# Kernel tuning notes

Measured on AMD Instinct MI355X. Metric: run time of the kernel, lower is better.

## Reference

```python
import jax, jax.numpy as jnp
import numpy as np
import math

N_EMBD = 1024
N_HEAD = 16
HEAD_DIM = N_EMBD // N_HEAD


def setup_inputs() -> dict:
    key = jax.random.key(0)
    k_x, k_w1, k_b1, k_w2, k_b2 = jax.random.split(key, 5)
    B, T = 2, 2048
    x = jax.random.normal(k_x, (B, T, N_EMBD), dtype=jnp.float32)
    # ln1: Linear(n_embd, 3*n_embd); weights stored as [in, out] for x @ W
    W_qkv = jax.random.normal(k_w1, (N_EMBD, 3 * N_EMBD), dtype=jnp.float32) * 0.02
    b_qkv = jax.random.normal(k_b1, (3 * N_EMBD,), dtype=jnp.float32) * 0.02
    # ln2: Linear(n_embd, n_embd)
    W_out = jax.random.normal(k_w2, (N_EMBD, N_EMBD), dtype=jnp.float32) * 0.02
    b_out = jax.random.normal(k_b2, (N_EMBD,), dtype=jnp.float32) * 0.02
    return {"x": x, "W_qkv": W_qkv, "b_qkv": b_qkv, "W_out": W_out, "b_out": b_out}


def reference(x, W_qkv, b_qkv, W_out, b_out):
    B, T, C = x.shape
    qkv = x @ W_qkv + b_qkv                      # [B,T,3C]
    q, k, v = jnp.split(qkv, 3, axis=-1)
    # reshape to heads: [B, H, T, D]
    def to_heads(t):
        return t.reshape(B, T, N_HEAD, HEAD_DIM).transpose(0, 2, 1, 3)
    Q, K, V = to_heads(q), to_heads(k), to_heads(v)
    # NOTE: scale is 1/sqrt(n_head), as in the source (not sqrt(head_dim));
    # NOTE: no causal mask is applied, faithfully matching the source forward.
    scale = 1.0 / math.sqrt(N_HEAD)
    scores = jnp.einsum('bhqd,bhkd->bhqk', Q, K) * scale  # [B,H,T,T]
    attn = jax.nn.softmax(scores, axis=-1)
    out = jnp.einsum('bhqk,bhkd->bhqd', attn, V)          # [B,H,T,D]
    out = out.transpose(0, 2, 1, 3).reshape(B, T, C)
    # dropout = 0.0 -> identity (eval mode)
    return out @ W_out + b_out
```

## Files before the change

kernel.cpp:

```cpp
#include <hip/hip_runtime.h>
#include <hip/hip_bf16.h>
#include <stdint.h>

typedef __bf16 bf16_t;
typedef __bf16 bf16x8 __attribute__((ext_vector_type(8)));
typedef float  f32x4  __attribute__((ext_vector_type(4)));

#define AS1 __attribute__((address_space(1)))
#define AS3 __attribute__((address_space(3)))

__device__ __forceinline__ void gload16(const bf16_t* g, char* l) {
  __builtin_amdgcn_global_load_lds((AS1 const void*)(uintptr_t)g, (AS3 void*)l, 16, 0, 0);
}
__device__ __forceinline__ int swz8(int r) { return (r & 7) ^ ((r >> 2) & 6); }

#define C2S 0.36067376022224085f

__global__ __launch_bounds__(256) void prep(
    const float* __restrict__ x, const float* __restrict__ Wqkv, const float* __restrict__ Wout,
    bf16_t* __restrict__ xb, bf16_t* __restrict__ wqkvT, bf16_t* __restrict__ woutT) {
  __shared__ float tile[32][33];
  const int bid = blockIdx.x, tid = threadIdx.x;
  if (bid < 4096) {
    const int i = bid * 256 + tid;
    float4 v = reinterpret_cast<const float4*>(x)[i];
    union { bf16_t h[4]; unsigned long long u; } r;
    r.h[0] = (bf16_t)v.x; r.h[1] = (bf16_t)v.y; r.h[2] = (bf16_t)v.z; r.h[3] = (bf16_t)v.w;
    reinterpret_cast<unsigned long long*>(xb)[i] = r.u;
    return;
  }
  const float* W; bf16_t* Wt; int N, tb;
  if (bid < 7168) { W = Wqkv; Wt = wqkvT; N = 3072; tb = bid - 4096; }
  else            { W = Wout; Wt = woutT; N = 1024; tb = bid - 7168; }
  const int kb = (tb & 31) * 32, nb = (tb >> 5) * 32;
  const int tx = tid & 31, ty = tid >> 5;
#pragma unroll
  for (int i = 0; i < 32; i += 8)
    tile[ty + i][tx] = W[(size_t)(kb + ty + i) * N + nb + tx];
  __syncthreads();
  const int r = tid >> 3;
  const int c0 = (tid & 7) * 4;
  union { bf16_t h4[4]; unsigned long long u; } pk;
#pragma unroll
  for (int j = 0; j < 4; ++j) pk.h4[j] = (bf16_t)tile[c0 + j][r];
  *reinterpret_cast<unsigned long long*>(&Wt[(size_t)(nb + r) * 1024 + kb + c0]) = pk.u;
}

__global__ __launch_bounds__(512) void gemm8(
    const bf16_t* __restrict__ A, const bf16_t* __restrict__ Bt,
    const float* __restrict__ bias,
    bf16_t* __restrict__ outb, bf16_t* __restrict__ vtb,
    int N, int K, int ldo) {
  __shared__ bf16_t lA[3][4096];
  __shared__ bf16_t lB[3][4096];
  const int tid = threadIdx.x;
  const int wave = tid >> 6, lane = tid & 63;
  const int lr = lane & 15, lg = lane >> 4;
  const int ntiles = N >> 7;
  int bm, bn;
  if (ntiles == 24) {
    const int xcd = blockIdx.x & 7, l = blockIdx.x >> 3;
    bm = (xcd >> 1) * 8 + (l & 7);
    bn = (xcd & 1) * 12 + (l >> 3);
  } else {
    const int bid = (blockIdx.x & 7) * ((int)gridDim.x >> 3) + (blockIdx.x >> 3);
    bn = bid % ntiles; bm = bid / ntiles;
  }
  const int m0 = bm * 128, n0 = bn * 128;
  const int wr = wave >> 2, wc = wave & 3;
  f32x4 acc[4][2] = {};

  const int srow = tid >> 2;
  const int scolb = ((tid & 3) << 4) ^ (((srow >> 1) & 3) << 4);
  const bf16_t* Asrc = A  + (size_t)(m0 + srow) * K + (scolb >> 1);
  const bf16_t* Bsrc = Bt + (size_t)(n0 + srow) * K + (scolb >> 1);
  auto stage = [&](int buf, int k0) {
    gload16(Asrc + k0, (char*)&lA[buf][0] + wave * 1024);
    gload16(Bsrc + k0, (char*)&lB[buf][0] + wave * 1024);
  };

  auto ldA = [&](const char* p, int mi) {
    const int row = wr * 64 + mi * 16 + lr;
    return *reinterpret_cast<const bf16x8*>(p + row * 64 + ((lg * 16) ^ (((row >> 1) & 3) << 4)));
  };
  auto ldB = [&](const char* p, int ni) {
    const int row = wc * 32 + ni * 16 + lr;
    return *reinterpret_cast<const bf16x8*>(p + row * 64 + ((lg * 16) ^ (((row >> 1) & 3) << 4)));
  };

  const int nt = K >> 5;
  stage(0, 0);
  stage(1, 32);
  int cur = 0, stg = 2;

  for (int t = 0; t < nt; ++t) {
    if (t + 2 < nt) {
      stage(stg, (t + 2) << 5);
      asm volatile("s_waitcnt vmcnt(4)" ::: "memory");
    } else if (t + 1 < nt) {
      asm volatile("s_waitcnt vmcnt(2)" ::: "memory");
    } else {
      asm volatile("s_waitcnt vmcnt(0)" ::: "memory");
    }
    __builtin_amdgcn_s_barrier();
    __builtin_amdgcn_sched_barrier(0);

    const char* pA = (const char*)&lA[cur][0];
    const char* pB = (const char*)&lB[cur][0];
    bf16x8 af[4], bfv[2];
#pragma unroll
    for (int mi = 0; mi < 4; ++mi) af[mi] = ldA(pA, mi);
    bfv[0] = ldB(pB, 0); bfv[1] = ldB(pB, 1);

    __builtin_amdgcn_s_setprio(1);
#pragma unroll
    for (int mi = 0; mi < 4; ++mi)
#pragma unroll
      for (int ni = 0; ni < 2; ++ni)
        acc[mi][ni] = __builtin_amdgcn_mfma_f32_16x16x32_bf16(af[mi], bfv[ni], acc[mi][ni], 0, 0, 0);
    __builtin_amdgcn_s_setprio(0);

    __builtin_amdgcn_sched_barrier(0);
    __builtin_amdgcn_s_barrier();
    cur = cur == 2 ? 0 : cur + 1;
    stg = stg == 2 ? 0 : stg + 1;
  }

#pragma unroll
  for (int mi = 0; mi < 4; ++mi) {
#pragma unroll
    for (int ni = 0; ni < 2; ++ni) {
      const int col = n0 + wc * 32 + ni * 16 + lr;
      const float bv = bias[col];
      const int rg0 = m0 + wr * 64 + mi * 16 + lg * 4;
      if (col >= 2048) {
        const int colv = col - 2048;
        const int dd = colv & 63, hh = colv >> 6;
        const int bb = rg0 >> 11, t = rg0 & 2047;
        union { bf16_t h4[4]; unsigned long long u; } pk;
#pragma unroll
        for (int r = 0; r < 4; ++r) pk.h4[r] = (bf16_t)(acc[mi][ni][r] + bv);
        *reinterpret_cast<unsigned long long*>(
            vtb + (size_t)(bb * 16 + hh) * 131072 + (size_t)dd * 2048 + t) = pk.u;
      } else {
        const float sc = (col < 1024) ? C2S : 1.f;
#pragma unroll
        for (int r = 0; r < 4; ++r) {
          const float v = (acc[mi][ni][r] + bv) * sc;
          outb[(size_t)(rg0 + r) * ldo + col] = (bf16_t)v;
        }
      }
    }
  }
}

__global__ __launch_bounds__(512) void attn_fwd(
    const bf16_t* __restrict__ qkv2,
    const bf16_t* __restrict__ vT,
    bf16_t* __restrict__ a0, bf16_t* __restrict__ a1,
    float* __restrict__ lbuf) {
  __shared__ bf16_t lds[4][8192];
  const int tid = threadIdx.x;
  const int wave = tid >> 6, lane = tid & 63;
  const int lr = lane & 15, lg = lane >> 4;
  const int id = blockIdx.x;
  const int xcd = id & 7, slot = id >> 3;
  const int bh = xcd * 4 + (slot & 3);
  const int rest = slot >> 2;
  const int qb = rest & 7, kvh = rest >> 3;
  const int b = bh >> 4, h = bh & 15;

  const int q0 = qb * 256 + wave * 32;
  const bf16_t* Qp = qkv2 + (size_t)(b * 2048 + q0) * 2048 + h * 64;
  bf16x8 qf[2][2];
#pragma unroll
  for (int hx = 0; hx < 2; ++hx) {
    qf[hx][0] = *reinterpret_cast<const bf16x8*>(Qp + (size_t)(hx * 16 + lr) * 2048 + lg * 8);
    qf[hx][1] = *reinterpret_cast<const bf16x8*>(Qp + (size_t)(hx * 16 + lr) * 2048 + 32 + lg * 8);
  }

  const int kr = tid >> 3;
  const int ks = (tid & 7) ^ swz8(kr);
  const bf16_t* Ksrc = qkv2 + (size_t)(b * 2048 + kvh * 1024 + kr) * 2048 + 1024 + h * 64 + ks * 8;
  const bf16_t* Vsrc = vT + (size_t)bh * 131072 + (size_t)kr * 2048 + kvh * 1024 + ks * 8;

  auto stage = [&](int buf, int kb) {
    char* base = (char*)&lds[buf][0] + wave * 1024;
    gload16(Ksrc + (size_t)kb * 131072, base);
    gload16(Vsrc + (size_t)kb * 64, base + 8192);
  };

  int kofs[4][2], vofs[4][2];
#pragma unroll
  for (int t = 0; t < 4; ++t) {
    const int kk = 32 * (t >> 1) + 8 * (lr >> 2) + 4 * (t & 1) + (lr & 3);
    const int sw = swz8(kk) << 4;
    kofs[t][0] = (kk << 7) + ((lg * 16) ^ sw);
    kofs[t][1] = (kk << 7) + ((64 + lg * 16) ^ sw);
  }
#pragma unroll
  for (int nc = 0; nc < 4; ++nc) {
    const int vr = nc * 16 + lr;
    const int sw = swz8(vr) << 4;
    vofs[nc][0] = 8192 + (vr << 7) + ((lg * 16) ^ sw);
    vofs[nc][1] = 8192 + (vr << 7) + ((64 + lg * 16) ^ sw);
  }

  f32x4 acc[2][4] = {};
  f32x4 accl[2] = {};
  bf16x8 ones;
#pragma unroll
  for (int j = 0; j < 8; ++j) ones[j] = (bf16_t)1.0f;

  stage(0, 0);
  stage(1, 1);

  for (int kb = 0; kb < 16; ++kb) {
    const int cur = kb & 3;
    if (kb + 2 < 16) {
      stage((kb + 2) & 3, kb + 2);
      asm volatile("s_waitcnt vmcnt(4)" ::: "memory");
    } else if (kb + 1 < 16) {
      asm volatile("s_waitcnt vmcnt(2)" ::: "memory");
    } else {
      asm volatile("s_waitcnt vmcnt(0)" ::: "memory");
    }
    __builtin_amdgcn_s_barrier();
    __builtin_amdgcn_sched_barrier(0);
    const char* bK = (const char*)&lds[cur][0];

    f32x4 s[2][4];
#pragma unroll
    for (int t = 0; t < 4; ++t) {
      const bf16x8 k0 = *reinterpret_cast<const bf16x8*>(bK + kofs[t][0]);
      const bf16x8 k1 = *reinterpret_cast<const bf16x8*>(bK + kofs[t][1]);
#pragma unroll
      for (int hx = 0; hx < 2; ++hx) {
        f32x4 z = {0.f, 0.f, 0.f, 0.f};
        z = __builtin_amdgcn_mfma_f32_16x16x32_bf16(k0, qf[hx][0], z, 0, 0, 0);
        s[hx][t] = __builtin_amdgcn_mfma_f32_16x16x32_bf16(k1, qf[hx][1], z, 0, 0, 0);
      }
    }

    bf16x8 pa[2][2];
#pragma unroll
    for (int hx = 0; hx < 2; ++hx) {
      float p[16];
#pragma unroll
      for (int t = 0; t < 4; ++t)
#pragma unroll
        for (int r = 0; r < 4; ++r)
          p[t * 4 + r] = __builtin_amdgcn_exp2f(s[hx][t][r]);
#pragma unroll
      for (int j = 0; j < 8; ++j) { pa[hx][0][j] = (bf16_t)p[j]; pa[hx][1][j] = (bf16_t)p[8 + j]; }
    }

    __builtin_amdgcn_s_setprio(1);
#pragma unroll
    for (int hx = 0; hx < 2; ++hx) {
      accl[hx] = __builtin_amdgcn_mfma_f32_16x16x32_bf16(pa[hx][0], ones, accl[hx], 0, 0, 0);
      accl[hx] = __builtin_amdgcn_mfma_f32_16x16x32_bf16(pa[hx][1], ones, accl[hx], 0, 0, 0);
    }
#pragma unroll
    for (int nc = 0; nc < 4; ++nc) {
      const bf16x8 v0 = *reinterpret_cast<const bf16x8*>(bK + vofs[nc][0]);
      const bf16x8 v1 = *reinterpret_cast<const bf16x8*>(bK + vofs[nc][1]);
#pragma unroll
      for (int hx = 0; hx < 2; ++hx) {
        acc[hx][nc] = __builtin_amdgcn_mfma_f32_16x16x32_bf16(pa[hx][0], v0, acc[hx][nc], 0, 0, 0);
        acc[hx][nc] = __builtin_amdgcn_mfma_f32_16x16x32_bf16(pa[hx][1], v1, acc[hx][nc], 0, 0, 0);
      }
    }
    __builtin_amdgcn_s_setprio(0);
  }

  bf16_t* ap = kvh ? a1 : a0;
#pragma unroll
  for (int hx = 0; hx < 2; ++hx) {
#pragma unroll
    for (int r = 0; r < 4; ++r) {
      const float lf = 1.f / accl[hx][r];
      const int qg = q0 + hx * 16 + lg * 4 + r;
      bf16_t* op = ap + (size_t)(b * 2048 + qg) * 1024 + h * 64 + lr;
#pragma unroll
      for (int nc = 0; nc < 4; ++nc) op[nc * 16] = (bf16_t)(acc[hx][nc][r] * lf);
      if (lr == 0)
        lbuf[(size_t)(kvh * 4096 + b * 2048 + qg) * 16 + h] = accl[hx][r];
    }
  }
}

__global__ __launch_bounds__(512) void gemm2m(
    const bf16_t* __restrict__ a0, const bf16_t* __restrict__ a1,
    const float* __restrict__ lbuf, const bf16_t* __restrict__ Bt,
    const float* __restrict__ bias, float* __restrict__ outf) {
  __shared__ bf16_t lA[2][2048];
  __shared__ bf16_t lB[2][4096];
  const int tid = threadIdx.x;
  const int wave = tid >> 6, lane = tid & 63;
  const int lr = lane & 15, lg = lane >> 4;
  const int bid = (blockIdx.x & 7) * 64 + (blockIdx.x >> 3);
  const int bm = bid >> 3, bn = bid & 7;
  const int m0 = bm * 64, n0 = bn * 128;
  const int wr = wave >> 2, wc = wave & 3;
  f32x4 acc[2][2] = {};

  const int srow = tid >> 2;
  const int scolb = ((tid & 3) << 4) ^ (((srow >> 1) & 3) << 4);
  const int scol = scolb >> 1;

  const bf16_t* pa0 = a0 + (size_t)(m0 + srow) * 1024 + scol;
  const bf16_t* pa1 = a1 + (size_t)(m0 + srow) * 1024 + scol;
  const float*  pl0 = lbuf + (size_t)(m0 + srow) * 16;
  const float*  pl1 = lbuf + (size_t)(4096 + m0 + srow) * 16;
  const bf16_t* pB0 = Bt + (size_t)(n0 + srow) * 1024 + scol;

  bf16x8 nA0 = {}, nA1 = {};
  float  nl0 = 1.f, nl1 = 1.f;
  if (tid < 256) {
    nA0 = *reinterpret_cast<const bf16x8*>(pa0);
    nA1 = *reinterpret_cast<const bf16x8*>(pa1);
    nl0 = pl0[0]; nl1 = pl1[0];
  }
  bf16x8 nB0v = *reinterpret_cast<const bf16x8*>(pB0);

  for (int t = 0; t < 32; ++t) {
    const int cur = t & 1;
    if (tid < 256) {
      const float inv = 1.f / (nl0 + nl1);
      const float w0 = nl0 * inv, w1 = nl1 * inv;
      bf16x8 mv;
#pragma unroll
      for (int j = 0; j < 8; ++j)
        mv[j] = (bf16_t)(w0 * (float)nA0[j] + w1 * (float)nA1[j]);
      *reinterpret_cast<bf16x8*>((char*)&lA[cur][0] + tid * 16) = mv;
    }
    *reinterpret_cast<bf16x8*>((char*)&lB[cur][0] + tid * 16) = nB0v;
    __syncthreads();

    if (t < 31) {
      const int k0 = (t + 1) * 32;
      const int h = k0 >> 6;
      if (tid < 256) {
        nA0 = *reinterpret_cast<const bf16x8*>(pa0 + k0);
        nA1 = *reinterpret_cast<const bf16x8*>(pa1 + k0);
        nl0 = pl0[h]; nl1 = pl1[h];
      }
      nB0v = *reinterpret_cast<const bf16x8*>(pB0 + k0);
    }

    const char* pA = (const char*)&lA[cur][0];
    const char* pB = (const char*)&lB[cur][0];
    bf16x8 af[2], bfv[2];
#pragma unroll
    for (int mi = 0; mi < 2; ++mi) {
      const int row = wr * 32 + mi * 16 + lr;
      af[mi] = *reinterpret_cast<const bf16x8*>(pA + row * 64 + ((lg * 16) ^ (((row >> 1) & 3) << 4)));
    }
#pragma unroll
    for (int ni = 0; ni < 2; ++ni) {
      const int row = wc * 32 + ni * 16 + lr;
      bfv[ni] = *reinterpret_cast<const bf16x8*>(pB + row * 64 + ((lg * 16) ^ (((row >> 1) & 3) << 4)));
    }
    __builtin_amdgcn_s_setprio(1);
#pragma unroll
    for (int mi = 0; mi < 2; ++mi)
#pragma unroll
      for (int ni = 0; ni < 2; ++ni)
        acc[mi][ni] = __builtin_amdgcn_mfma_f32_16x16x32_bf16(af[mi], bfv[ni], acc[mi][ni], 0, 0, 0);
    __builtin_amdgcn_s_setprio(0);
    __syncthreads();
  }

#pragma unroll
  for (int mi = 0; mi < 2; ++mi)
#pragma unroll
    for (int ni = 0; ni < 2; ++ni) {
      const int col = n0 + wc * 32 + ni * 16 + lr;
      const float bv = bias[col];
      const int rg0 = m0 + wr * 32 + mi * 16 + lg * 4;
#pragma unroll
      for (int r = 0; r < 4; ++r)
        outf[(size_t)(rg0 + r) * 1024 + col] = acc[mi][ni][r] + bv;
    }
}

extern "C" void kernel_launch(void* const* d_in, const int* in_sizes, int n_in,
                              void* d_out, int out_size, void* d_ws, size_t ws_size,
                              hipStream_t stream) {
  (void)in_sizes; (void)n_in; (void)out_size; (void)ws_size;
  const float* x    = (const float*)d_in[0];
  const float* Wqkv = (const float*)d_in[1];
  const float* bqkv = (const float*)d_in[2];
  const float* Wout = (const float*)d_in[3];
  const float* bout = (const float*)d_in[4];
  float* out = (float*)d_out;

  char* ws = (char*)d_ws;
  bf16_t* xb    = (bf16_t*)(ws);
  bf16_t* a0    = (bf16_t*)(ws);
  bf16_t* wqkvT = (bf16_t*)(ws + 8388608);
  bf16_t* woutT = (bf16_t*)(ws + 14680064);
  bf16_t* qkv2  = (bf16_t*)(ws + 16777216);
  bf16_t* vT    = (bf16_t*)(ws + 33554432);
  bf16_t* a1    = (bf16_t*)(ws + 41943040);
  float*  lbuf  = (float*)(ws + 50331648);

  prep<<<8192, 256, 0, stream>>>(x, Wqkv, Wout, xb, wqkvT, woutT);
  gemm8<<<768, 512, 0, stream>>>(xb, wqkvT, bqkv, qkv2, vT, 3072, 1024, 2048);
  attn_fwd<<<512, 512, 0, stream>>>(qkv2, vT, a0, a1, lbuf);
  gemm2m<<<512, 512, 0, stream>>>(a0, a1, lbuf, woutT, bout, out);
}
```

Measured before the change: 110.6 us.

## Fuse x fp32-to-bf16 conversion into QKV GEMM A-tile loading

Removes the separate pass that converts x to bf16 in the prep kernel. The QKV GEMM now reads fp32 x directly into registers, converts it to bf16, and writes it into swizzled LDS, interleaved with async global-to-LDS loads of B. This drops a 16MB read plus 8MB write of intermediate data and shrinks the prep launch. In exchange, A loads go through registers instead of direct-to-LDS, each fp32 x row is re-read by every N-tile block (24 of them), and the waitcnt pipeline scheme becomes more intricate.

```diff
diff --git a/kernel.cpp b/kernel.cpp
--- a/kernel.cpp
+++ b/kernel.cpp
@@ -17,21 +17,13 @@
 #define C2S 0.36067376022224085f
 
 __global__ __launch_bounds__(256) void prep(
-    const float* __restrict__ x, const float* __restrict__ Wqkv, const float* __restrict__ Wout,
-    bf16_t* __restrict__ xb, bf16_t* __restrict__ wqkvT, bf16_t* __restrict__ woutT) {
+    const float* __restrict__ Wqkv, const float* __restrict__ Wout,
+    bf16_t* __restrict__ wqkvT, bf16_t* __restrict__ woutT) {
   __shared__ float tile[32][33];
   const int bid = blockIdx.x, tid = threadIdx.x;
-  if (bid < 4096) {
-    const int i = bid * 256 + tid;
-    float4 v = reinterpret_cast<const float4*>(x)[i];
-    union { bf16_t h[4]; unsigned long long u; } r;
-    r.h[0] = (bf16_t)v.x; r.h[1] = (bf16_t)v.y; r.h[2] = (bf16_t)v.z; r.h[3] = (bf16_t)v.w;
-    reinterpret_cast<unsigned long long*>(xb)[i] = r.u;
-    return;
-  }
   const float* W; bf16_t* Wt; int N, tb;
-  if (bid < 7168) { W = Wqkv; Wt = wqkvT; N = 3072; tb = bid - 4096; }
-  else            { W = Wout; Wt = woutT; N = 1024; tb = bid - 7168; }
+  if (bid < 3072) { W = Wqkv; Wt = wqkvT; N = 3072; tb = bid; }
+  else            { W = Wout; Wt = woutT; N = 1024; tb = bid - 3072; }
   const int kb = (tb & 31) * 32, nb = (tb >> 5) * 32;
   const int tx = tid & 31, ty = tid >> 5;
 #pragma unroll
@@ -47,7 +39,7 @@
 }
 
 __global__ __launch_bounds__(512) void gemm8(
-    const bf16_t* __restrict__ A, const bf16_t* __restrict__ Bt,
+    const float* __restrict__ X, const bf16_t* __restrict__ Bt,
     const float* __restrict__ bias,
     bf16_t* __restrict__ outb, bf16_t* __restrict__ vtb,
     int N, int K, int ldo) {
@@ -70,12 +62,21 @@
   const int wr = wave >> 2, wc = wave & 3;
   f32x4 acc[4][2] = {};
 
+  const int arow = tid >> 2;
+  const int ac0 = (tid & 3) * 8;
+  const float* pAx = X + (size_t)(m0 + arow) * (size_t)K + ac0;
+  const int adst = arow * 64 + (((tid & 3) << 4) ^ (((arow >> 1) & 3) << 4));
+  auto cvtwr = [&](int buf, const f32x4& lo, const f32x4& hi) {
+    bf16x8 v;
+    v[0] = (bf16_t)lo[0]; v[1] = (bf16_t)lo[1]; v[2] = (bf16_t)lo[2]; v[3] = (bf16_t)lo[3];
+    v[4] = (bf16_t)hi[0]; v[5] = (bf16_t)hi[1]; v[6] = (bf16_t)hi[2]; v[7] = (bf16_t)hi[3];
+    *reinterpret_cast<bf16x8*>((char*)&lA[buf][0] + adst) = v;
+  };
+
   const int srow = tid >> 2;
   const int scolb = ((tid & 3) << 4) ^ (((srow >> 1) & 3) << 4);
-  const bf16_t* Asrc = A  + (size_t)(m0 + srow) * K + (scolb >> 1);
   const bf16_t* Bsrc = Bt + (size_t)(n0 + srow) * K + (scolb >> 1);
-  auto stage = [&](int buf, int k0) {
-    gload16(Asrc + k0, (char*)&lA[buf][0] + wave * 1024);
+  auto stageB = [&](int buf, int k0) {
     gload16(Bsrc + k0, (char*)&lB[buf][0] + wave * 1024);
   };
 
@@ -89,19 +90,35 @@
   };
 
   const int nt = K >> 5;
-  stage(0, 0);
-  stage(1, 32);
-  int cur = 0, stg = 2;
+  {
+    f32x4 lo = *reinterpret_cast<const f32x4*>(pAx);
+    f32x4 hi = *reinterpret_cast<const f32x4*>(pAx + 4);
+    cvtwr(0, lo, hi);
+    lo = *reinterpret_cast<const f32x4*>(pAx + 32);
+    hi = *reinterpret_cast<const f32x4*>(pAx + 36);
+    cvtwr(1, lo, hi);
+  }
+  stageB(0, 0);
+  stageB(1, 32);
+  f32x4 nlo = *reinterpret_cast<const f32x4*>(pAx + 64);
+  f32x4 nhi = *reinterpret_cast<const f32x4*>(pAx + 68);
+  stageB(2, 64);
+  asm volatile("s_waitcnt lgkmcnt(0)" ::: "memory");
 
   for (int t = 0; t < nt; ++t) {
-    if (t + 2 < nt) {
-      stage(stg, (t + 2) << 5);
-      asm volatile("s_waitcnt vmcnt(4)" ::: "memory");
-    } else if (t + 1 < nt) {
-      asm volatile("s_waitcnt vmcnt(2)" ::: "memory");
-    } else {
-      asm volatile("s_waitcnt vmcnt(0)" ::: "memory");
-    }
+    const int cur = t % 3;
+    if (t >= 1 && t + 1 < nt) {
+      cvtwr((t + 1) % 3, nlo, nhi);
+      asm volatile("s_waitcnt lgkmcnt(0)" ::: "memory");
+      if (t + 2 < nt) {
+        nlo = *reinterpret_cast<const f32x4*>(pAx + (t + 2) * 32);
+        nhi = *reinterpret_cast<const f32x4*>(pAx + (t + 2) * 32 + 4);
+        stageB((t + 2) % 3, (t + 2) * 32);
+      }
+    }
+    if (t + 2 < nt)      asm volatile("s_waitcnt vmcnt(4)" ::: "memory");
+    else if (t + 1 < nt) asm volatile("s_waitcnt vmcnt(1)" ::: "memory");
+    else                 asm volatile("s_waitcnt vmcnt(0)" ::: "memory");
     __builtin_amdgcn_s_barrier();
     __builtin_amdgcn_sched_barrier(0);
 
@@ -122,8 +139,6 @@
 
     __builtin_amdgcn_sched_barrier(0);
     __builtin_amdgcn_s_barrier();
-    cur = cur == 2 ? 0 : cur + 1;
-    stg = stg == 2 ? 0 : stg + 1;
   }
 
 #pragma unroll
@@ -397,7 +412,6 @@
   float* out = (float*)d_out;
 
   char* ws = (char*)d_ws;
-  bf16_t* xb    = (bf16_t*)(ws);
   bf16_t* a0    = (bf16_t*)(ws);
   bf16_t* wqkvT = (bf16_t*)(ws + 8388608);
   bf16_t* woutT = (bf16_t*)(ws + 14680064);
@@ -406,8 +420,8 @@
   bf16_t* a1    = (bf16_t*)(ws + 41943040);
   float*  lbuf  = (float*)(ws + 50331648);
 
-  prep<<<8192, 256, 0, stream>>>(x, Wqkv, Wout, xb, wqkvT, woutT);
-  gemm8<<<768, 512, 0, stream>>>(xb, wqkvT, bqkv, qkv2, vT, 3072, 1024, 2048);
+  prep<<<4096, 256, 0, stream>>>(Wqkv, Wout, wqkvT, woutT);
+  gemm8<<<768, 512, 0, stream>>>(x, wqkvT, bqkv, qkv2, vT, 3072, 1024, 2048);
   attn_fwd<<<512, 512, 0, stream>>>(qkv2, vT, a0, a1, lbuf);
   gemm2m<<<512, 512, 0, stream>>>(a0, a1, lbuf, woutT, bout, out);
 }
```

Measured after the change: 111.4 us. About the same (+0.7%).
